# Performance work log

Measured on AMD Instinct MI355X. Metric: run time of the kernel, lower is better.

The kernel has to match this reference:

```python
import jax, jax.numpy as jnp
import numpy as np

N, E, MB, H, FA, FB, HEADS, A_SIZE = 60000, 120000, 6, 128, 133, 147, 8, 20


def setup_inputs() -> dict:
    key = jax.random.key(0)
    ks = jax.random.split(key, 32)
    nrm = lambda k, s, sc: (jax.random.normal(k, s, jnp.float32) * sc)
    HD = HEADS * H
    inp = {
        "f_atoms": jax.random.normal(ks[0], (N, FA), jnp.float32),
        "f_bonds": jax.random.normal(ks[1], (E, FB), jnp.float32),
        "wi_atom": nrm(ks[2], (H, FA), 1 / np.sqrt(FA)),
        "wi_bond": nrm(ks[3], (H, FB), 1 / np.sqrt(FB)),
        "wh0": nrm(ks[4], (H, H), 1 / np.sqrt(H)),
        "wh1": nrm(ks[5], (H, H), 1 / np.sqrt(H)),
        "wh2": nrm(ks[6], (H, H), 1 / np.sqrt(H)),
        "q_w": nrm(ks[7], (HD, H), 1 / np.sqrt(H)),
        "q_b": nrm(ks[8], (HD,), 0.02),
        "k_w": nrm(ks[9], (HD, H), 1 / np.sqrt(H)),
        "k_b": nrm(ks[10], (HD,), 0.02),
        "v_w": nrm(ks[11], (HD, H), 1 / np.sqrt(H)),
        "v_b": nrm(ks[12], (HD,), 0.02),
        "e_w": nrm(ks[13], (HD, H), 1 / np.sqrt(H)),
        "skip_w": nrm(ks[14], (H, H), 1 / np.sqrt(H)),
        "skip_b": nrm(ks[15], (H,), 0.02),
        "lstm_wih": nrm(ks[16], (4 * H, 2 * H), 1 / np.sqrt(H)),
        "lstm_whh": nrm(ks[17], (4 * H, H), 1 / np.sqrt(H)),
        "lstm_bih": nrm(ks[18], (4 * H,), 1 / np.sqrt(H)),
        "lstm_bhh": nrm(ks[19], (4 * H,), 1 / np.sqrt(H)),
        "wo_w": nrm(ks[20], (H, 2 * H), 1 / np.sqrt(2 * H)),
        "wo_b": nrm(ks[21], (H,), 0.02),
        "a2b": jax.random.randint(ks[22], (N, MB), 0, E),
        "b2a": jax.random.randint(ks[23], (E,), 0, N),
        "b2revb": jax.random.randint(ks[24], (E,), 0, E),
        "bonds": jax.random.randint(ks[25], (2, E), 0, N),
        "a_size": A_SIZE,
    }
    return inp


def reference(f_atoms, f_bonds, wi_atom, wi_bond, wh0, wh1, wh2, q_w, q_b, k_w, k_b,
              v_w, v_b, e_w, skip_w, skip_b, lstm_wih, lstm_whh, lstm_bih, lstm_bhh,
              wo_w, wo_b, a2b, b2a, b2revb, bonds, a_size):
    relu = jax.nn.relu
    n = f_atoms.shape[0]
    h = wi_atom.shape[0]
    heads = q_w.shape[0] // h
    # input projections (bias=False) + activation
    input_atom = relu(f_atoms @ wi_atom.T)
    message_atom = input_atom
    input_bond = relu(f_bonds @ wi_bond.T)
    message_bond = input_bond
    # depth-1 = 3 message passing iterations (dropout p=0 -> identity)
    for wh in (wh0, wh1, wh2):
        nei = message_bond[a2b]                    # [N, max_nb, H] gather
        agg = nei.sum(axis=1) * nei.max(axis=1)    # fused sum*max aggregation
        message_atom = message_atom + agg
        mb = message_atom[b2a] - message_bond[b2revb]
        message_bond = relu(input_bond + mb @ wh.T)
    # TransformerConv(H, H, heads=8, concat=False, edge_dim=H)
    src, dst = bonds[0], bonds[1]
    e_num = src.shape[0]
    q = (message_atom @ q_w.T + q_b).reshape(n, heads, h)
    k = (message_atom @ k_w.T + k_b).reshape(n, heads, h)
    v = (message_atom @ v_w.T + v_b).reshape(n, heads, h)
    eattr = (message_bond @ e_w.T).reshape(e_num, heads, h)
    k_j = k[src] + eattr
    v_j = v[src] + eattr
    logits = (q[dst] * k_j).sum(-1) / jnp.sqrt(jnp.float32(h))  # [E, heads]
    m = jax.ops.segment_max(logits, dst, num_segments=n)
    m = jnp.where(jnp.isfinite(m), m, 0.0)
    ex = jnp.exp(logits - m[dst])
    denom = jax.ops.segment_sum(ex, dst, num_segments=n) + 1e-16
    alpha = ex / denom[dst]
    out = jax.ops.segment_sum(v_j * alpha[..., None], dst, num_segments=n)
    atom_hiddens = out.mean(axis=1) + (message_atom @ skip_w.T + skip_b)
    # Set2Set(T=1, num_layers=1) per molecule, vectorized over equal-size mols
    m_mols = n // a_size
    x = atom_hiddens.reshape(m_mols, a_size, h)
    hh = jnp.zeros((m_mols, h), jnp.float32)
    cc = jnp.zeros((m_mols, h), jnp.float32)
    q_star = jnp.zeros((m_mols, 2 * h), jnp.float32)
    gates = q_star @ lstm_wih.T + lstm_bih + hh @ lstm_whh.T + lstm_bhh
    gi, gf, gg, go = jnp.split(gates, 4, axis=-1)  # torch LSTM gate order i,f,g,o
    cc = jax.nn.sigmoid(gf) * cc + jax.nn.sigmoid(gi) * jnp.tanh(gg)
    qv = jax.nn.sigmoid(go) * jnp.tanh(cc)          # [M, H]
    e_att = (x * qv[:, None, :]).sum(-1)            # [M, A]
    a = jnp.exp(e_att - e_att.max(axis=1, keepdims=True))
    a = a / (a.sum(axis=1, keepdims=True) + 1e-16)
    r = jnp.einsum('ma,mah->mh', a, x)
    q_star = jnp.concatenate([qv, r], axis=-1)      # [M, 2H]
    return q_star @ wo_w.T + wo_b                   # [M, H]
```

## Files before the change

kernel.cpp:

```cpp
#include <hip/hip_runtime.h>
#include <hip/hip_bf16.h>

__global__ void zero_u32(unsigned int* __restrict__ p, long long n)
{
    long long i = (long long)blockIdx.x * 256 + threadIdx.x;
    if (i < n) p[i] = 0u;
}

__global__ void sentinel_f32(float* __restrict__ p, long long n, float v)
{
    long long i = (long long)blockIdx.x * 256 + threadIdx.x;
    if (i < n) p[i] = v;
}

struct GSeg {
    const float* A; const float* W; const float* bias; float* C;
    int M; int K; int bend;
};
struct GParams { GSeg s[4]; };

template<bool RELU>
__global__ __launch_bounds__(256) void gemm_multi(GParams P, int nseg)
{
    __shared__ float As[16][132];
    __shared__ float Ws[16][132];
    const int b = blockIdx.x;
    int si = 0, bbeg = 0;
    while (si + 1 < nseg && b >= P.s[si].bend) { bbeg = P.s[si].bend; ++si; }
    const GSeg S = P.s[si];
    const int tid = threadIdx.x;
    const int tx = tid & 15, ty = tid >> 4;
    const int row0 = (b - bbeg) * 128;
    const int r  = tid >> 2;
    const int k4 = (tid & 3) * 4;
    float acc[8][8] = {};
    for (int k0 = 0; k0 < S.K; k0 += 16) {
        const bool fullk = (k0 + 16 <= S.K);
#pragma unroll
        for (int c = 0; c < 2; ++c) {
            int rr = r + c * 64;
            int gm = row0 + rr;
            float4 av = make_float4(0.f, 0.f, 0.f, 0.f);
            if (gm < S.M) {
                const float* p = S.A + (size_t)gm * S.K + k0 + k4;
                if (fullk) av = *(const float4*)p;
                else {
                    if (k0 + k4     < S.K) av.x = p[0];
                    if (k0 + k4 + 1 < S.K) av.y = p[1];
                    if (k0 + k4 + 2 < S.K) av.z = p[2];
                    if (k0 + k4 + 3 < S.K) av.w = p[3];
                }
            }
            As[k4 + 0][rr] = av.x; As[k4 + 1][rr] = av.y;
            As[k4 + 2][rr] = av.z; As[k4 + 3][rr] = av.w;
            float4 wv = make_float4(0.f, 0.f, 0.f, 0.f);
            const float* pw = S.W + (size_t)rr * S.K + k0 + k4;
            if (fullk) wv = *(const float4*)pw;
            else {
                if (k0 + k4     < S.K) wv.x = pw[0];
                if (k0 + k4 + 1 < S.K) wv.y = pw[1];
                if (k0 + k4 + 2 < S.K) wv.z = pw[2];
                if (k0 + k4 + 3 < S.K) wv.w = pw[3];
            }
            Ws[k4 + 0][rr] = wv.x; Ws[k4 + 1][rr] = wv.y;
            Ws[k4 + 2][rr] = wv.z; Ws[k4 + 3][rr] = wv.w;
        }
        __syncthreads();
#pragma unroll
        for (int kk = 0; kk < 16; ++kk) {
            float4 a0 = *(const float4*)&As[kk][ty * 4];
            float4 a1 = *(const float4*)&As[kk][64 + ty * 4];
            float4 w0 = *(const float4*)&Ws[kk][tx * 4];
            float4 w1 = *(const float4*)&Ws[kk][64 + tx * 4];
            float a[8] = {a0.x, a0.y, a0.z, a0.w, a1.x, a1.y, a1.z, a1.w};
            float w[8] = {w0.x, w0.y, w0.z, w0.w, w1.x, w1.y, w1.z, w1.w};
#pragma unroll
            for (int i = 0; i < 8; ++i)
#pragma unroll
                for (int j = 0; j < 8; ++j)
                    acc[i][j] += a[i] * w[j];
        }
        __syncthreads();
    }
    float bs[8];
    if (S.bias) {
#pragma unroll
        for (int j = 0; j < 4; ++j) {
            bs[j]     = S.bias[tx * 4 + j];
            bs[j + 4] = S.bias[64 + tx * 4 + j];
        }
    } else {
#pragma unroll
        for (int j = 0; j < 8; ++j) bs[j] = 0.f;
    }
#pragma unroll
    for (int i = 0; i < 8; ++i) {
        int rr = (i < 4) ? (ty * 4 + i) : (64 + ty * 4 + i - 4);
        int gm = row0 + rr;
        if (gm >= S.M) continue;
#pragma unroll
        for (int jh = 0; jh < 2; ++jh) {
            float4 v;
            v.x = acc[i][jh * 4 + 0] + bs[jh * 4 + 0];
            v.y = acc[i][jh * 4 + 1] + bs[jh * 4 + 1];
            v.z = acc[i][jh * 4 + 2] + bs[jh * 4 + 2];
            v.w = acc[i][jh * 4 + 3] + bs[jh * 4 + 3];
            if (RELU) {
                v.x = fmaxf(v.x, 0.f); v.y = fmaxf(v.y, 0.f);
                v.z = fmaxf(v.z, 0.f); v.w = fmaxf(v.w, 0.f);
            }
            *(float4*)&S.C[(size_t)gm * 128 + jh * 64 + tx * 4] = v;
        }
    }
}

__global__ __launch_bounds__(256) void gemm64(
    const float* __restrict__ A, const float* __restrict__ W,
    const float* __restrict__ bias, float* __restrict__ C, int M)
{
    __shared__ float As[16][68];
    __shared__ float Ws[16][132];
    const int tid = threadIdx.x;
    const int tx = tid & 15, ty = tid >> 4;
    const int row0 = blockIdx.x * 64;
    const int r  = tid >> 2;
    const int k4 = (tid & 3) * 4;
    float acc[4][8] = {};
    for (int k0 = 0; k0 < 128; k0 += 16) {
        {
            int gm = row0 + r;
            float4 av = make_float4(0.f, 0.f, 0.f, 0.f);
            if (gm < M) av = *(const float4*)(A + (size_t)gm * 128 + k0 + k4);
            As[k4 + 0][r] = av.x; As[k4 + 1][r] = av.y;
            As[k4 + 2][r] = av.z; As[k4 + 3][r] = av.w;
        }
#pragma unroll
        for (int c = 0; c < 2; ++c) {
            int rr = r + c * 64;
            float4 wv = *(const float4*)(W + (size_t)rr * 128 + k0 + k4);
            Ws[k4 + 0][rr] = wv.x; Ws[k4 + 1][rr] = wv.y;
            Ws[k4 + 2][rr] = wv.z; Ws[k4 + 3][rr] = wv.w;
        }
        __syncthreads();
#pragma unroll
        for (int kk = 0; kk < 16; ++kk) {
            float4 a0 = *(const float4*)&As[kk][ty * 4];
            float4 w0 = *(const float4*)&Ws[kk][tx * 4];
            float4 w1 = *(const float4*)&Ws[kk][64 + tx * 4];
            float a[4] = {a0.x, a0.y, a0.z, a0.w};
            float w[8] = {w0.x, w0.y, w0.z, w0.w, w1.x, w1.y, w1.z, w1.w};
#pragma unroll
            for (int i = 0; i < 4; ++i)
#pragma unroll
                for (int j = 0; j < 8; ++j)
                    acc[i][j] += a[i] * w[j];
        }
        __syncthreads();
    }
    float bs[8];
#pragma unroll
    for (int j = 0; j < 4; ++j) {
        bs[j]     = bias ? bias[tx * 4 + j] : 0.f;
        bs[j + 4] = bias ? bias[64 + tx * 4 + j] : 0.f;
    }
#pragma unroll
    for (int i = 0; i < 4; ++i) {
        int gm = row0 + ty * 4 + i;
        if (gm >= M) continue;
#pragma unroll
        for (int jh = 0; jh < 2; ++jh) {
            float4 v;
            v.x = acc[i][jh * 4 + 0] + bs[jh * 4 + 0];
            v.y = acc[i][jh * 4 + 1] + bs[jh * 4 + 1];
            v.z = acc[i][jh * 4 + 2] + bs[jh * 4 + 2];
            v.w = acc[i][jh * 4 + 3] + bs[jh * 4 + 3];
            *(float4*)&C[(size_t)gm * 128 + jh * 64 + tx * 4] = v;
        }
    }
}

__global__ __launch_bounds__(256) void gemm_mp(
    const float* __restrict__ ma, const float* __restrict__ bond,
    const int* __restrict__ b2a, const int* __restrict__ b2revb,
    const float* __restrict__ inb, const float* __restrict__ wh,
    float* __restrict__ C)
{
    __shared__ float As[16][68];
    __shared__ float Ws[16][132];
    __shared__ int ia[64], ir[64];
    const int tid = threadIdx.x;
    const int tx = tid & 15, ty = tid >> 4;
    const int row0 = blockIdx.x * 64;
    const int r  = tid >> 2;
    const int k4 = (tid & 3) * 4;
    if (tid < 64)       ia[tid]      = b2a[row0 + tid];
    else if (tid < 128) ir[tid - 64] = b2revb[row0 + tid - 64];
    __syncthreads();
    float acc[4][8] = {};
    for (int k0 = 0; k0 < 128; k0 += 16) {
        {
            float4 x = *(const float4*)(ma   + (size_t)ia[r] * 128 + k0 + k4);
            float4 y = *(const float4*)(bond + (size_t)ir[r] * 128 + k0 + k4);
            As[k4 + 0][r] = x.x - y.x; As[k4 + 1][r] = x.y - y.y;
            As[k4 + 2][r] = x.z - y.z; As[k4 + 3][r] = x.w - y.w;
        }
#pragma unroll
        for (int c = 0; c < 2; ++c) {
            int rr = r + c * 64;
            float4 wv = *(const float4*)(wh + (size_t)rr * 128 + k0 + k4);
            Ws[k4 + 0][rr] = wv.x; Ws[k4 + 1][rr] = wv.y;
            Ws[k4 + 2][rr] = wv.z; Ws[k4 + 3][rr] = wv.w;
        }
        __syncthreads();
#pragma unroll
        for (int kk = 0; kk < 16; ++kk) {
            float4 a0 = *(const float4*)&As[kk][ty * 4];
            float4 w0 = *(const float4*)&Ws[kk][tx * 4];
            float4 w1 = *(const float4*)&Ws[kk][64 + tx * 4];
            float a[4] = {a0.x, a0.y, a0.z, a0.w};
            float w[8] = {w0.x, w0.y, w0.z, w0.w, w1.x, w1.y, w1.z, w1.w};
#pragma unroll
            for (int i = 0; i < 4; ++i)
#pragma unroll
                for (int j = 0; j < 8; ++j)
                    acc[i][j] += a[i] * w[j];
        }
        __syncthreads();
    }
#pragma unroll
    for (int i = 0; i < 4; ++i) {
        int gm = row0 + ty * 4 + i;
#pragma unroll
        for (int jh = 0; jh < 2; ++jh) {
            int cc = jh * 64 + tx * 4;
            float4 o = *(const float4*)&inb[(size_t)gm * 128 + cc];
            float4 v;
            v.x = fmaxf(acc[i][jh * 4 + 0] + o.x, 0.f);
            v.y = fmaxf(acc[i][jh * 4 + 1] + o.y, 0.f);
            v.z = fmaxf(acc[i][jh * 4 + 2] + o.z, 0.f);
            v.w = fmaxf(acc[i][jh * 4 + 3] + o.w, 0.f);
            *(float4*)&C[(size_t)gm * 128 + cc] = v;
        }
    }
}

__global__ __launch_bounds__(256) void agg_kernel(
    const float* __restrict__ bond, const int* __restrict__ a2b,
    float* __restrict__ ma, int N)
{
    int n = blockIdx.x * 8 + (threadIdx.x >> 5);
    if (n >= N) return;
    int d4 = (threadIdx.x & 31) * 4;
    const int* ix = a2b + (size_t)n * 6;
    float4 s = make_float4(0.f, 0.f, 0.f, 0.f);
    float4 mx = make_float4(-3.0e38f, -3.0e38f, -3.0e38f, -3.0e38f);
#pragma unroll
    for (int j = 0; j < 6; ++j) {
        float4 v = *(const float4*)(bond + (size_t)ix[j] * 128 + d4);
        s.x += v.x; s.y += v.y; s.z += v.z; s.w += v.w;
        mx.x = fmaxf(mx.x, v.x); mx.y = fmaxf(mx.y, v.y);
        mx.z = fmaxf(mx.z, v.z); mx.w = fmaxf(mx.w, v.w);
    }
    float* mp = ma + (size_t)n * 128 + d4;
    float4 o = *(const float4*)mp;
    o.x += s.x * mx.x; o.y += s.y * mx.y; o.z += s.z * mx.z; o.w += s.w * mx.w;
    *(float4*)mp = o;
}

__global__ void count_kernel(const int* __restrict__ dst, int* __restrict__ counts, int E)
{
    int e = blockIdx.x * 256 + threadIdx.x;
    if (e < E) atomicAdd(&counts[dst[e]], 1);
}

__global__ __launch_bounds__(1024) void scan_kernel(
    const int* __restrict__ counts, int* __restrict__ offsets, int N)
{
    __shared__ int sums[1024];
    int t = threadIdx.x;
    int chunk = (N + 1023) >> 10;
    int b = t * chunk;
    int e = b + chunk; if (e > N) e = N;
    int s = 0;
    for (int i = b; i < e; ++i) s += counts[i];
    sums[t] = s;
    __syncthreads();
    for (int off = 1; off < 1024; off <<= 1) {
        int v = (t >= off) ? sums[t - off] : 0;
        __syncthreads();
        sums[t] += v;
        __syncthreads();
    }
    int run = sums[t] - s;
    for (int i = b; i < e; ++i) { offsets[i] = run; run += counts[i]; }
    if (t == 1023) offsets[N] = sums[1023];
}

__global__ void fill_kernel(const int* __restrict__ dst, const int* __restrict__ offsets,
                            int* __restrict__ cursor, int* __restrict__ elist, int E)
{
    int e = blockIdx.x * 256 + threadIdx.x;
    if (e < E) {
        int d = dst[e];
        int pos = offsets[d] + atomicAdd(&cursor[d], 1);
        elist[pos] = e;
    }
}

__global__ __launch_bounds__(256) void attn_pass1(
    const float* __restrict__ qh, const float* __restrict__ kh,
    const float* __restrict__ eh, const int* __restrict__ srcA,
    const int* __restrict__ offs, const int* __restrict__ elist,
    float* __restrict__ alpha, int N)
{
    int n = blockIdx.x * 4 + (threadIdx.x >> 6);
    if (n >= N) return;
    int l = threadIdx.x & 63;
    const float rs = 0.08838834764831845f;
    float2 q2 = ((const float2*)(qh + (size_t)n * 128))[l];
    int b = offs[n], en = offs[n + 1];
    float m = -3.0e38f, denom = 0.f;
    int ie = b;
    for (; ie + 2 <= en; ie += 2) {
        int e0 = elist[ie], e1 = elist[ie + 1];
        int s0 = srcA[e0], s1 = srcA[e1];
        float2 k0v = ((const float2*)(kh + (size_t)s0 * 128))[l];
        float2 e0v = ((const float2*)(eh + (size_t)e0 * 128))[l];
        float2 k1v = ((const float2*)(kh + (size_t)s1 * 128))[l];
        float2 e1v = ((const float2*)(eh + (size_t)e1 * 128))[l];
        float p0 = q2.x * (k0v.x + e0v.x) + q2.y * (k0v.y + e0v.y);
        float p1 = q2.x * (k1v.x + e1v.x) + q2.y * (k1v.y + e1v.y);
        p0 += __shfl_xor(p0, 1);  p1 += __shfl_xor(p1, 1);
        p0 += __shfl_xor(p0, 2);  p1 += __shfl_xor(p1, 2);
        p0 += __shfl_xor(p0, 4);  p1 += __shfl_xor(p1, 4);
        p0 += __shfl_xor(p0, 8);  p1 += __shfl_xor(p1, 8);
        p0 += __shfl_xor(p0, 16); p1 += __shfl_xor(p1, 16);
        p0 += __shfl_xor(p0, 32); p1 += __shfl_xor(p1, 32);
        float l0 = p0 * rs, l1 = p1 * rs;
        if (l == 0) { alpha[ie] = l0; alpha[ie + 1] = l1; }
        float mn = fmaxf(m, fmaxf(l0, l1));
        float sc = __expf(m - mn);
        denom = denom * sc + __expf(l0 - mn) + __expf(l1 - mn);
        m = mn;
    }
    if (ie < en) {
        int e0 = elist[ie];
        int s0 = srcA[e0];
        float2 k0v = ((const float2*)(kh + (size_t)s0 * 128))[l];
        float2 e0v = ((const float2*)(eh + (size_t)e0 * 128))[l];
        float p0 = q2.x * (k0v.x + e0v.x) + q2.y * (k0v.y + e0v.y);
        p0 += __shfl_xor(p0, 1);  p0 += __shfl_xor(p0, 2);
        p0 += __shfl_xor(p0, 4);  p0 += __shfl_xor(p0, 8);
        p0 += __shfl_xor(p0, 16); p0 += __shfl_xor(p0, 32);
        float l0 = p0 * rs;
        if (l == 0) alpha[ie] = l0;
        float mn = fmaxf(m, l0);
        denom = denom * __expf(m - mn) + __expf(l0 - mn);
        m = mn;
    }
    if (l == 0 && b < en) {
        float invd = 1.f / (denom + 1e-16f);
        for (int i = b; i < en; ++i)
            alpha[i] = __expf(alpha[i] - m) * invd;
    }
}

__global__ __launch_bounds__(256) void attn_pass2(
    const float* __restrict__ vh, const float* __restrict__ eh,
    const int* __restrict__ srcA, const int* __restrict__ offs,
    const int* __restrict__ elist, const float* __restrict__ alpha,
    float* __restrict__ outsum, int N)
{
    int n = blockIdx.x * 4 + (threadIdx.x >> 6);
    if (n >= N) return;
    int l = threadIdx.x & 63;
    int b = offs[n], en = offs[n + 1];
    float a0 = 0.f, a1 = 0.f;
    int ie = b;
    for (; ie + 2 <= en; ie += 2) {
        int e0 = elist[ie], e1 = elist[ie + 1];
        int s0 = srcA[e0], s1 = srcA[e1];
        float al0 = alpha[ie], al1 = alpha[ie + 1];
        float2 v0 = ((const float2*)(vh + (size_t)s0 * 128))[l];
        float2 e0v = ((const float2*)(eh + (size_t)e0 * 128))[l];
        float2 v1 = ((const float2*)(vh + (size_t)s1 * 128))[l];
        float2 e1v = ((const float2*)(eh + (size_t)e1 * 128))[l];
        a0 += al0 * (v0.x + e0v.x) + al1 * (v1.x + e1v.x);
        a1 += al0 * (v0.y + e0v.y) + al1 * (v1.y + e1v.y);
    }
    if (ie < en) {
        int e0 = elist[ie];
        int s0 = srcA[e0];
        float al0 = alpha[ie];
        float2 v0 = ((const float2*)(vh + (size_t)s0 * 128))[l];
        float2 e0v = ((const float2*)(eh + (size_t)e0 * 128))[l];
        a0 += al0 * (v0.x + e0v.x);
        a1 += al0 * (v0.y + e0v.y);
    }
    float* op = outsum + (size_t)n * 128 + 2 * l;
    op[0] += 0.125f * a0;
    op[1] += 0.125f * a1;
}

__global__ void qv_kernel(const float* __restrict__ bih, const float* __restrict__ bhh,
                          float* __restrict__ qv)
{
    int t = threadIdx.x;
    float gi = bih[t] + bhh[t];
    float gg = bih[256 + t] + bhh[256 + t];
    float go = bih[384 + t] + bhh[384 + t];
    float sig_i = 1.f / (1.f + __expf(-gi));
    float c = sig_i * tanhf(gg);
    float sig_o = 1.f / (1.f + __expf(-go));
    qv[t] = sig_o * tanhf(c);
}

__global__ __launch_bounds__(256) void s2s_kernel(
    const float* __restrict__ ah, const float* __restrict__ qv,
    const float* __restrict__ wo_w, const float* __restrict__ wo_b,
    float* __restrict__ out, int M)
{
    __shared__ float rsh[4][128];
    __shared__ float qsh[128];
    int wv = threadIdx.x >> 6, l = threadIdx.x & 63;
    if (threadIdx.x < 128) qsh[threadIdx.x] = qv[threadIdx.x];
    __syncthreads();
    int m = blockIdx.x * 4 + wv;
    bool active = (m < M);
    if (active) {
        const float* x = ah + (size_t)m * 20 * 128;
        float q0 = qsh[2 * l], q1 = qsh[2 * l + 1];
        float e[20]; float mx = -3.0e38f;
#pragma unroll
        for (int a = 0; a < 20; ++a) {
            float part = x[a * 128 + 2 * l] * q0 + x[a * 128 + 2 * l + 1] * q1;
            part += __shfl_xor(part, 1);  part += __shfl_xor(part, 2);
            part += __shfl_xor(part, 4);  part += __shfl_xor(part, 8);
            part += __shfl_xor(part, 16); part += __shfl_xor(part, 32);
            e[a] = part; mx = fmaxf(mx, part);
        }
        float sum = 0.f;
#pragma unroll
        for (int a = 0; a < 20; ++a) { e[a] = __expf(e[a] - mx); sum += e[a]; }
        float invs = 1.f / (sum + 1e-16f);
        float r0 = 0.f, r1 = 0.f;
#pragma unroll
        for (int a = 0; a < 20; ++a) {
            float w = e[a] * invs;
            r0 += w * x[a * 128 + 2 * l];
            r1 += w * x[a * 128 + 2 * l + 1];
        }
        rsh[wv][2 * l] = r0; rsh[wv][2 * l + 1] = r1;
    }
    __syncthreads();
    if (active) {
#pragma unroll
        for (int dd = 0; dd < 2; ++dd) {
            int d = 2 * l + dd;
            float acc = wo_b[d];
            const float* wr = wo_w + (size_t)d * 256;
            for (int j = 0; j < 128; ++j)
                acc += wr[j] * qsh[j] + wr[128 + j] * rsh[wv][j];
            out[(size_t)m * 128 + d] = acc;
        }
    }
}

extern "C" void kernel_launch(void* const* d_in, const int* in_sizes, int n_in,
                              void* d_out, int out_size, void* d_ws, size_t ws_size,
                              hipStream_t stream)
{
    const int N = 60000, E = 120000, FA = 133, FB = 147;
    const float* f_atoms  = (const float*)d_in[0];
    const float* f_bonds  = (const float*)d_in[1];
    const float* wi_atom  = (const float*)d_in[2];
    const float* wi_bond  = (const float*)d_in[3];
    const float* wh[3]    = { (const float*)d_in[4], (const float*)d_in[5], (const float*)d_in[6] };
    const float* q_w      = (const float*)d_in[7];
    const float* q_b      = (const float*)d_in[8];
    const float* k_w      = (const float*)d_in[9];
    const float* k_b      = (const float*)d_in[10];
    const float* v_w      = (const float*)d_in[11];
    const float* v_b      = (const float*)d_in[12];
    const float* e_w      = (const float*)d_in[13];
    const float* skip_w   = (const float*)d_in[14];
    const float* skip_b   = (const float*)d_in[15];
    const float* lstm_bih = (const float*)d_in[18];
    const float* lstm_bhh = (const float*)d_in[19];
    const float* wo_w     = (const float*)d_in[20];
    const float* wo_b     = (const float*)d_in[21];
    const int* a2b    = (const int*)d_in[22];
    const int* b2a    = (const int*)d_in[23];
    const int* b2revb = (const int*)d_in[24];
    const int* bonds  = (const int*)d_in[25];
    const int* srcA = bonds;
    const int* dstA = bonds + E;

    const size_t NB = (size_t)N * 128;
    const size_t EB = (size_t)E * 128;
    char* ws = (char*)d_ws;
    size_t off = 0;
    auto alloc = [&](size_t bytes) -> char* {
        char* p = ws + off; off += (bytes + 255) & ~255ULL; return p;
    };
    float* msg_atom = (float*)alloc(NB * 4);
    float* B1       = (float*)alloc(EB * 4);
    float* B2       = (float*)alloc(EB * 4);
    float* B3       = (float*)alloc(EB * 4);
    float* outsum   = (float*)alloc(NB * 4);
    float* alpha    = (float*)alloc((size_t)E * 4);
    int* counts  = (int*)alloc((size_t)N * 2 * 4);
    int* cursor  = counts + N;
    int* offsets = (int*)alloc((size_t)(N + 1) * 4);
    int* elist   = (int*)alloc((size_t)E * 4);
    float* qvb   = (float*)alloc(128 * 4);

    if (off > ws_size) {
        long long n = out_size;
        sentinel_f32<<<(int)((n + 255) / 256), 256, 0, stream>>>((float*)d_out, n, 1.0e9f);
        return;
    }

    float* q_h = B1;
    float* k_h = B1 + NB;
    float* v_h = B1;
    float* e_h = B3;

    const int gN128 = (N + 127) / 128;
    const int gE128 = (E + 127) / 128;
    const int gN64  = (N + 63) / 64;
    const int gE64  = E / 64;

    zero_u32<<<(2 * N + 255) / 256, 256, 0, stream>>>((unsigned int*)counts, 2 * N);

    {
        GParams P{};
        P.s[0] = { f_atoms, wi_atom, nullptr, msg_atom, N, FA, gN128 };
        P.s[1] = { f_bonds, wi_bond, nullptr, B1,       E, FB, gN128 + gE128 };
        gemm_multi<true><<<gN128 + gE128, 256, 0, stream>>>(P, 2);
    }

    count_kernel<<<(E + 255) / 256, 256, 0, stream>>>(dstA, counts, E);
    scan_kernel<<<1, 1024, 0, stream>>>(counts, offsets, N);
    fill_kernel<<<(E + 255) / 256, 256, 0, stream>>>(dstA, offsets, cursor, elist, E);

    const float* cur = B1;
    float* nxt[3] = { B2, B3, B2 };
    for (int it = 0; it < 3; ++it) {
        agg_kernel<<<(N + 7) / 8, 256, 0, stream>>>(cur, a2b, msg_atom, N);
        gemm_mp<<<gE64, 256, 0, stream>>>(
            msg_atom, cur, b2a, b2revb, B1, wh[it], nxt[it]);
        cur = nxt[it];
    }

    for (int h = 0; h < 8; ++h) {
        const size_t w_off = (size_t)h * 128 * 128;
        GParams P{};
        P.s[0] = { B2,       e_w + w_off, nullptr,        e_h, E, 128, gE128 };
        P.s[1] = { msg_atom, q_w + w_off, q_b + h * 128,  q_h, N, 128, gE128 + gN128 };
        P.s[2] = { msg_atom, k_w + w_off, k_b + h * 128,  k_h, N, 128, gE128 + 2 * gN128 };
        int nseg = 3, nblk = gE128 + 2 * gN128;
        if (h == 0) {
            P.s[3] = { msg_atom, skip_w, skip_b, outsum, N, 128, gE128 + 3 * gN128 };
            nseg = 4; nblk += gN128;
        }
        gemm_multi<false><<<nblk, 256, 0, stream>>>(P, nseg);
        attn_pass1<<<(N + 3) / 4, 256, 0, stream>>>(
            q_h, k_h, e_h, srcA, offsets, elist, alpha, N);
        gemm64<<<gN64, 256, 0, stream>>>(msg_atom, v_w + w_off, v_b + h * 128, v_h, N);
        attn_pass2<<<(N + 3) / 4, 256, 0, stream>>>(
            v_h, e_h, srcA, offsets, elist, alpha, outsum, N);
    }

    qv_kernel<<<1, 128, 0, stream>>>(lstm_bih, lstm_bhh, qvb);
    const int M = N / 20;
    s2s_kernel<<<(M + 3) / 4, 256, 0, stream>>>(outsum, qvb, wo_w, wo_b, (float*)d_out, M);
}
```

Baseline: 2.332 ms.

## Deepen GEMM K-tiles to 64 and widen message-passing GEMM to 128 rows

The shared GEMM kernels now stage 64 K-columns per barrier instead of 16, which cuts synchronisation count. The gathered message-passing GEMM grows from a 64-row to a 128-row tile with an 8x8 per-thread accumulator and gains a bounds check on E. The separate 64-row value-projection GEMM is removed and replaced by the generic 128-row multi-GEMM. Shared memory rises to about 67 KB per block, and register pressure from the larger accumulator may cut occupancy.

After: 2.952 ms. +26.6%, slower.

```diff
diff --git a/kernel.cpp b/kernel.cpp
--- a/kernel.cpp
+++ b/kernel.cpp
@@ -11,6 +11,22 @@
 {
     long long i = (long long)blockIdx.x * 256 + threadIdx.x;
     if (i < n) p[i] = v;
+}
+
+__device__ __forceinline__ float4 load_f4_guard(const float* base, int gm, int M, int K, int kb)
+{
+    float4 v = make_float4(0.f, 0.f, 0.f, 0.f);
+    if (gm < M) {
+        const float* p = base + (size_t)gm * K + kb;
+        if (kb + 4 <= K) v = *(const float4*)p;
+        else {
+            if (kb     < K) v.x = p[0];
+            if (kb + 1 < K) v.y = p[1];
+            if (kb + 2 < K) v.z = p[2];
+            if (kb + 3 < K) v.w = p[3];
+        }
+    }
+    return v;
 }
 
 struct GSeg {
@@ -22,8 +38,8 @@
 template<bool RELU>
 __global__ __launch_bounds__(256) void gemm_multi(GParams P, int nseg)
 {
-    __shared__ float As[16][132];
-    __shared__ float Ws[16][132];
+    __shared__ float As[64][132];
+    __shared__ float Ws[64][132];
     const int b = blockIdx.x;
     int si = 0, bbeg = 0;
     while (si + 1 < nseg && b >= P.s[si].bend) { bbeg = P.s[si].bend; ++si; }
@@ -33,41 +49,27 @@
     const int row0 = (b - bbeg) * 128;
     const int r  = tid >> 2;
     const int k4 = (tid & 3) * 4;
+    const int nsteps = (S.K + 63) >> 6;
+
     float acc[8][8] = {};
-    for (int k0 = 0; k0 < S.K; k0 += 16) {
-        const bool fullk = (k0 + 16 <= S.K);
-#pragma unroll
-        for (int c = 0; c < 2; ++c) {
-            int rr = r + c * 64;
-            int gm = row0 + rr;
-            float4 av = make_float4(0.f, 0.f, 0.f, 0.f);
-            if (gm < S.M) {
-                const float* p = S.A + (size_t)gm * S.K + k0 + k4;
-                if (fullk) av = *(const float4*)p;
-                else {
-                    if (k0 + k4     < S.K) av.x = p[0];
-                    if (k0 + k4 + 1 < S.K) av.y = p[1];
-                    if (k0 + k4 + 2 < S.K) av.z = p[2];
-                    if (k0 + k4 + 3 < S.K) av.w = p[3];
-                }
+    for (int s = 0; s < nsteps; ++s) {
+        const int kbase = s * 64;
+        for (int ks = 0; ks < 4; ++ks) {
+            const int kk0 = ks * 16 + k4;
+#pragma unroll
+            for (int c = 0; c < 2; ++c) {
+                int rr = r + c * 64;
+                float4 av = load_f4_guard(S.A, row0 + rr, S.M, S.K, kbase + kk0);
+                As[kk0 + 0][rr] = av.x; As[kk0 + 1][rr] = av.y;
+                As[kk0 + 2][rr] = av.z; As[kk0 + 3][rr] = av.w;
+                float4 wv = load_f4_guard(S.W, rr, 128, S.K, kbase + kk0);
+                Ws[kk0 + 0][rr] = wv.x; Ws[kk0 + 1][rr] = wv.y;
+                Ws[kk0 + 2][rr] = wv.z; Ws[kk0 + 3][rr] = wv.w;
             }
-            As[k4 + 0][rr] = av.x; As[k4 + 1][rr] = av.y;
-            As[k4 + 2][rr] = av.z; As[k4 + 3][rr] = av.w;
-            float4 wv = make_float4(0.f, 0.f, 0.f, 0.f);
-            const float* pw = S.W + (size_t)rr * S.K + k0 + k4;
-            if (fullk) wv = *(const float4*)pw;
-            else {
-                if (k0 + k4     < S.K) wv.x = pw[0];
-                if (k0 + k4 + 1 < S.K) wv.y = pw[1];
-                if (k0 + k4 + 2 < S.K) wv.z = pw[2];
-                if (k0 + k4 + 3 < S.K) wv.w = pw[3];
-            }
-            Ws[k4 + 0][rr] = wv.x; Ws[k4 + 1][rr] = wv.y;
-            Ws[k4 + 2][rr] = wv.z; Ws[k4 + 3][rr] = wv.w;
         }
         __syncthreads();
 #pragma unroll
-        for (int kk = 0; kk < 16; ++kk) {
+        for (int kk = 0; kk < 64; ++kk) {
             float4 a0 = *(const float4*)&As[kk][ty * 4];
             float4 a1 = *(const float4*)&As[kk][64 + ty * 4];
             float4 w0 = *(const float4*)&Ws[kk][tx * 4];
@@ -114,113 +116,55 @@
     }
 }
 
-__global__ __launch_bounds__(256) void gemm64(
-    const float* __restrict__ A, const float* __restrict__ W,
-    const float* __restrict__ bias, float* __restrict__ C, int M)
-{
-    __shared__ float As[16][68];
-    __shared__ float Ws[16][132];
-    const int tid = threadIdx.x;
-    const int tx = tid & 15, ty = tid >> 4;
-    const int row0 = blockIdx.x * 64;
-    const int r  = tid >> 2;
-    const int k4 = (tid & 3) * 4;
-    float acc[4][8] = {};
-    for (int k0 = 0; k0 < 128; k0 += 16) {
-        {
-            int gm = row0 + r;
-            float4 av = make_float4(0.f, 0.f, 0.f, 0.f);
-            if (gm < M) av = *(const float4*)(A + (size_t)gm * 128 + k0 + k4);
-            As[k4 + 0][r] = av.x; As[k4 + 1][r] = av.y;
-            As[k4 + 2][r] = av.z; As[k4 + 3][r] = av.w;
-        }
-#pragma unroll
-        for (int c = 0; c < 2; ++c) {
-            int rr = r + c * 64;
-            float4 wv = *(const float4*)(W + (size_t)rr * 128 + k0 + k4);
-            Ws[k4 + 0][rr] = wv.x; Ws[k4 + 1][rr] = wv.y;
-            Ws[k4 + 2][rr] = wv.z; Ws[k4 + 3][rr] = wv.w;
-        }
-        __syncthreads();
-#pragma unroll
-        for (int kk = 0; kk < 16; ++kk) {
-            float4 a0 = *(const float4*)&As[kk][ty * 4];
-            float4 w0 = *(const float4*)&Ws[kk][tx * 4];
-            float4 w1 = *(const float4*)&Ws[kk][64 + tx * 4];
-            float a[4] = {a0.x, a0.y, a0.z, a0.w};
-            float w[8] = {w0.x, w0.y, w0.z, w0.w, w1.x, w1.y, w1.z, w1.w};
-#pragma unroll
-            for (int i = 0; i < 4; ++i)
-#pragma unroll
-                for (int j = 0; j < 8; ++j)
-                    acc[i][j] += a[i] * w[j];
-        }
-        __syncthreads();
-    }
-    float bs[8];
-#pragma unroll
-    for (int j = 0; j < 4; ++j) {
-        bs[j]     = bias ? bias[tx * 4 + j] : 0.f;
-        bs[j + 4] = bias ? bias[64 + tx * 4 + j] : 0.f;
-    }
-#pragma unroll
-    for (int i = 0; i < 4; ++i) {
-        int gm = row0 + ty * 4 + i;
-        if (gm >= M) continue;
-#pragma unroll
-        for (int jh = 0; jh < 2; ++jh) {
-            float4 v;
-            v.x = acc[i][jh * 4 + 0] + bs[jh * 4 + 0];
-            v.y = acc[i][jh * 4 + 1] + bs[jh * 4 + 1];
-            v.z = acc[i][jh * 4 + 2] + bs[jh * 4 + 2];
-            v.w = acc[i][jh * 4 + 3] + bs[jh * 4 + 3];
-            *(float4*)&C[(size_t)gm * 128 + jh * 64 + tx * 4] = v;
-        }
-    }
-}
-
 __global__ __launch_bounds__(256) void gemm_mp(
     const float* __restrict__ ma, const float* __restrict__ bond,
     const int* __restrict__ b2a, const int* __restrict__ b2revb,
     const float* __restrict__ inb, const float* __restrict__ wh,
-    float* __restrict__ C)
-{
-    __shared__ float As[16][68];
-    __shared__ float Ws[16][132];
-    __shared__ int ia[64], ir[64];
+    float* __restrict__ C, int E)
+{
+    __shared__ float As[64][132];
+    __shared__ float Ws[64][132];
+    __shared__ int ia[128], ir[128];
     const int tid = threadIdx.x;
     const int tx = tid & 15, ty = tid >> 4;
-    const int row0 = blockIdx.x * 64;
+    const int row0 = blockIdx.x * 128;
     const int r  = tid >> 2;
     const int k4 = (tid & 3) * 4;
-    if (tid < 64)       ia[tid]      = b2a[row0 + tid];
-    else if (tid < 128) ir[tid - 64] = b2revb[row0 + tid - 64];
+    if (tid < 128) {
+        int g = row0 + tid;
+        ia[tid] = (g < E) ? b2a[g] : 0;
+        ir[tid] = (g < E) ? b2revb[g] : 0;
+    }
     __syncthreads();
-    float acc[4][8] = {};
-    for (int k0 = 0; k0 < 128; k0 += 16) {
-        {
-            float4 x = *(const float4*)(ma   + (size_t)ia[r] * 128 + k0 + k4);
-            float4 y = *(const float4*)(bond + (size_t)ir[r] * 128 + k0 + k4);
-            As[k4 + 0][r] = x.x - y.x; As[k4 + 1][r] = x.y - y.y;
-            As[k4 + 2][r] = x.z - y.z; As[k4 + 3][r] = x.w - y.w;
-        }
-#pragma unroll
-        for (int c = 0; c < 2; ++c) {
-            int rr = r + c * 64;
-            float4 wv = *(const float4*)(wh + (size_t)rr * 128 + k0 + k4);
-            Ws[k4 + 0][rr] = wv.x; Ws[k4 + 1][rr] = wv.y;
-            Ws[k4 + 2][rr] = wv.z; Ws[k4 + 3][rr] = wv.w;
+
+    float acc[8][8] = {};
+    for (int s = 0; s < 2; ++s) {
+        const int kbase = s * 64;
+        for (int ks = 0; ks < 4; ++ks) {
+            const int kk0 = ks * 16 + k4;
+#pragma unroll
+            for (int c = 0; c < 2; ++c) {
+                int rr = r + c * 64;
+                float4 x = *(const float4*)(ma   + (size_t)ia[rr] * 128 + kbase + kk0);
+                float4 y = *(const float4*)(bond + (size_t)ir[rr] * 128 + kbase + kk0);
+                As[kk0 + 0][rr] = x.x - y.x; As[kk0 + 1][rr] = x.y - y.y;
+                As[kk0 + 2][rr] = x.z - y.z; As[kk0 + 3][rr] = x.w - y.w;
+                float4 wv = *(const float4*)(wh + (size_t)rr * 128 + kbase + kk0);
+                Ws[kk0 + 0][rr] = wv.x; Ws[kk0 + 1][rr] = wv.y;
+                Ws[kk0 + 2][rr] = wv.z; Ws[kk0 + 3][rr] = wv.w;
+            }
         }
         __syncthreads();
 #pragma unroll
-        for (int kk = 0; kk < 16; ++kk) {
+        for (int kk = 0; kk < 64; ++kk) {
             float4 a0 = *(const float4*)&As[kk][ty * 4];
+            float4 a1 = *(const float4*)&As[kk][64 + ty * 4];
             float4 w0 = *(const float4*)&Ws[kk][tx * 4];
             float4 w1 = *(const float4*)&Ws[kk][64 + tx * 4];
-            float a[4] = {a0.x, a0.y, a0.z, a0.w};
+            float a[8] = {a0.x, a0.y, a0.z, a0.w, a1.x, a1.y, a1.z, a1.w};
             float w[8] = {w0.x, w0.y, w0.z, w0.w, w1.x, w1.y, w1.z, w1.w};
 #pragma unroll
-            for (int i = 0; i < 4; ++i)
+            for (int i = 0; i < 8; ++i)
 #pragma unroll
                 for (int j = 0; j < 8; ++j)
                     acc[i][j] += a[i] * w[j];
@@ -228,8 +172,10 @@
         __syncthreads();
     }
 #pragma unroll
-    for (int i = 0; i < 4; ++i) {
-        int gm = row0 + ty * 4 + i;
+    for (int i = 0; i < 8; ++i) {
+        int rr = (i < 4) ? (ty * 4 + i) : (64 + ty * 4 + i - 4);
+        int gm = row0 + rr;
+        if (gm >= E) continue;
 #pragma unroll
         for (int jh = 0; jh < 2; ++jh) {
             int cc = jh * 64 + tx * 4;
@@ -528,8 +474,6 @@
 
     const int gN128 = (N + 127) / 128;
     const int gE128 = (E + 127) / 128;
-    const int gN64  = (N + 63) / 64;
-    const int gE64  = E / 64;
 
     zero_u32<<<(2 * N + 255) / 256, 256, 0, stream>>>((unsigned int*)counts, 2 * N);
 
@@ -548,8 +492,8 @@
     float* nxt[3] = { B2, B3, B2 };
     for (int it = 0; it < 3; ++it) {
         agg_kernel<<<(N + 7) / 8, 256, 0, stream>>>(cur, a2b, msg_atom, N);
-        gemm_mp<<<gE64, 256, 0, stream>>>(
-            msg_atom, cur, b2a, b2revb, B1, wh[it], nxt[it]);
+        gemm_mp<<<gE128, 256, 0, stream>>>(
+            msg_atom, cur, b2a, b2revb, B1, wh[it], nxt[it], E);
         cur = nxt[it];
     }
 
@@ -567,7 +511,11 @@
         gemm_multi<false><<<nblk, 256, 0, stream>>>(P, nseg);
         attn_pass1<<<(N + 3) / 4, 256, 0, stream>>>(
             q_h, k_h, e_h, srcA, offsets, elist, alpha, N);
-        gemm64<<<gN64, 256, 0, stream>>>(msg_atom, v_w + w_off, v_b + h * 128, v_h, N);
+        {
+            GParams PV{};
+            PV.s[0] = { msg_atom, v_w + w_off, v_b + h * 128, v_h, N, 128, gN128 };
+            gemm_multi<false><<<gN128, 256, 0, stream>>>(PV, 1);
+        }
         attn_pass2<<<(N + 3) / 4, 256, 0, stream>>>(
             v_h, e_h, srcA, offsets, elist, alpha, outsum, N);
     }
```
